# Kernel tuning notes

Measured on AMD Instinct MI355X. Metric: run time of the kernel, lower is better.

## Reference

```python
import jax, jax.numpy as jnp
import numpy as np

D_MODEL, N_LAYERS, NUM_CLASSES = 768, 4, 10
D_INNER = 2 * D_MODEL          # expand_factor=2
D_STATE = 16
D_CONV = 4
DT_RANK = (D_MODEL + 15) // 16  # ceil(d_model/16) = 48
B, L = 8, 2048
EPS = 1e-5


def setup_inputs() -> dict:
    key = jax.random.key(0)
    ks = jax.random.split(key, 16)
    s = 0.02
    inp = {
        'x': jax.random.normal(ks[0], (B, L, D_MODEL), jnp.float32),
        'labels': jax.random.randint(ks[1], (B,), 0, NUM_CLASSES, jnp.int64),
        # stacked per-layer params
        'in_proj_w': jax.random.normal(ks[2], (N_LAYERS, 2 * D_INNER, D_MODEL), jnp.float32) * s,
        'conv_w': jax.random.normal(ks[3], (N_LAYERS, D_INNER, 1, D_CONV), jnp.float32) * s,
        'conv_b': jnp.zeros((N_LAYERS, D_INNER), jnp.float32),
        'x_proj_w': jax.random.normal(ks[4], (N_LAYERS, DT_RANK + 2 * D_STATE, D_INNER), jnp.float32) * s,
        'dt_w': jax.random.normal(ks[5], (N_LAYERS, D_INNER, DT_RANK), jnp.float32) * s,
        'dt_b': jax.random.uniform(ks[6], (N_LAYERS, D_INNER), jnp.float32, -4.0, -2.0),
        'A_log': jnp.broadcast_to(jnp.log(jnp.arange(1, D_STATE + 1, dtype=jnp.float32)),
                                  (N_LAYERS, D_INNER, D_STATE)).copy(),
        'D_param': jnp.ones((N_LAYERS, D_INNER), jnp.float32),
        'out_proj_w': jax.random.normal(ks[7], (N_LAYERS, D_MODEL, D_INNER), jnp.float32) * s,
        'norm_w': jnp.ones((N_LAYERS, D_MODEL), jnp.float32),
        'normf_w': jnp.ones((D_MODEL,), jnp.float32),
        'cls_w': jax.random.normal(ks[8], (NUM_CLASSES, D_MODEL), jnp.float32) * s,
        'cls_b': jnp.zeros((NUM_CLASSES,), jnp.float32),
    }
    return inp


def rmsnorm(x, w):
    return x * jax.lax.rsqrt(jnp.mean(x * x, axis=-1, keepdims=True) + EPS) * w


def causal_dw_conv1d(x, w, b):
    # x: (B, L, ED), w: (ED, 1, K) depthwise, causal left padding
    y = jax.lax.conv_general_dilated(
        x.swapaxes(1, 2), w, window_strides=(1,), padding=[(D_CONV - 1, 0)],
        feature_group_count=D_INNER, dimension_numbers=('NCH', 'OIH', 'NCH'))
    return (y + b[:, None]).swapaxes(1, 2)


def selective_scan(xin, delta, Bm, Cm, A, Dp):
    # xin/delta: (B,L,ED), Bm/Cm: (B,L,N), A: (ED,N), Dp: (ED,)
    def step(h, t):
        d_t, B_t, C_t, x_t = t                      # (B,ED),(B,N),(B,N),(B,ED)
        dA = jnp.exp(d_t[..., None] * A)            # (B,ED,N)
        dBx = (d_t * x_t)[..., None] * B_t[:, None, :]
        h = dA * h + dBx
        y = jnp.einsum('ben,bn->be', h, C_t)
        return h, y

    h0 = jnp.zeros((xin.shape[0], D_INNER, D_STATE), xin.dtype)
    xs = (delta.swapaxes(0, 1), Bm.swapaxes(0, 1), Cm.swapaxes(0, 1), xin.swapaxes(0, 1))
    _, ys = jax.lax.scan(step, h0, xs)              # ys: (L,B,ED)
    return ys.swapaxes(0, 1) + xin * Dp


def mamba_block(x, in_w, cw, cb, xw, dtw, dtb, A_log, Dp, ow):
    xz = jnp.einsum('bld,ed->ble', x, in_w)         # (B,L,2*ED)
    xin, z = jnp.split(xz, 2, axis=-1)
    xin = jax.nn.silu(causal_dw_conv1d(xin, cw, cb))
    dbc = jnp.einsum('ble,fe->blf', xin, xw)
    delta_r = dbc[..., :DT_RANK]
    Bm = dbc[..., DT_RANK:DT_RANK + D_STATE]
    Cm = dbc[..., DT_RANK + D_STATE:]
    delta = jax.nn.softplus(jnp.einsum('blr,er->ble', delta_r, dtw) + dtb)
    A = -jnp.exp(A_log)
    y = selective_scan(xin, delta, Bm, Cm, A, Dp)
    y = y * jax.nn.silu(z)
    return jnp.einsum('ble,de->bld', y, ow)


def forward(x, labels, in_proj_w, conv_w, conv_b, x_proj_w, dt_w, dt_b,
            A_log, D_param, out_proj_w, norm_w, normf_w, cls_w, cls_b):
    h = x
    for i in range(N_LAYERS):
        h = h + mamba_block(rmsnorm(h, norm_w[i]), in_proj_w[i], conv_w[i], conv_b[i],
                            x_proj_w[i], dt_w[i], dt_b[i], A_log[i], D_param[i], out_proj_w[i])
    h = rmsnorm(h, normf_w)
    pooled = jnp.mean(h, axis=1)                    # (B, d_model)
    logits = pooled @ cls_w.T + cls_b               # (B, num_classes)
    logp = jax.nn.log_softmax(logits, axis=-1)
    loss = -jnp.mean(jnp.take_along_axis(logp, labels[:, None], axis=-1))
    return logits, loss


def reference(x, labels, in_proj_w, conv_w, conv_b, x_proj_w, dt_w, dt_b,
              A_log, D_param, out_proj_w, norm_w, normf_w, cls_w, cls_b):
    return forward(x, labels, in_proj_w, conv_w, conv_b, x_proj_w, dt_w, dt_b,
                   A_log, D_param, out_proj_w, norm_w, normf_w, cls_w, cls_b)
```

## Files before the change

### kernel.cpp

```cpp
#include <hip/hip_runtime.h>
#include <hip/hip_bf16.h>
#include <math.h>

#define MTOK 16384
#define DM   768
#define DI   1536
#define DS   16
#define RNK  48
#define LSEQ 2048
#define NBATCH 8
#define EPSV 1e-5f
#define CHK  16
#define CLEN (LSEQ / CHK)
#define BM 128
#define BN 128
#define BK 32
#define KSPLIT 8
#define EPS_STRIDE 72

typedef __hip_bfloat16 bf16;
typedef __attribute__((ext_vector_type(8))) short short8;
typedef __attribute__((ext_vector_type(4))) float floatx4;

__device__ __forceinline__ float b2f(bf16 v){ return __bfloat162float(v); }
__device__ __forceinline__ bf16  f2b(float v){ return __float2bfloat16(v); }
__device__ __forceinline__ float u2f(unsigned short u){
    union { unsigned int i; float f; } v; v.i = ((unsigned int)u) << 16; return v.f;
}
__device__ __forceinline__ unsigned pack_bf2(float a, float b){
    bf16 ta = f2b(a), tb = f2b(b);
    return (unsigned)(*(unsigned short*)&ta) | ((unsigned)(*(unsigned short*)&tb) << 16);
}
__device__ __forceinline__ float silu_f(float x){
    return x * __builtin_amdgcn_rcpf(1.f + __expf(-x));
}
__device__ __forceinline__ void gload_lds16(const void* g, void* l) {
    __builtin_amdgcn_global_load_lds(
        (const __attribute__((address_space(1))) void*)g,
        (__attribute__((address_space(3))) void*)l, 16, 0, 0);
}

__global__ __launch_bounds__(256) void cvt_kernel(
    const float* __restrict__ x, bf16* __restrict__ h, int n)
{
    int i = (blockIdx.x * 256 + threadIdx.x) * 4;
    if (i < n) {
        const float4 v = *(const float4*)(x + i);
        uint2 o;
        o.x = pack_bf2(v.x, v.y);
        o.y = pack_bf2(v.z, v.w);
        *(uint2*)((unsigned short*)h + i) = o;
    }
}

__global__ __launch_bounds__(256) void rmsnorm_kernel(
    const bf16* __restrict__ in, const float* __restrict__ w,
    bf16* __restrict__ out, float* __restrict__ rs_out)
{
    const int row  = blockIdx.x * 4 + (threadIdx.x >> 6);
    const int lane = threadIdx.x & 63;
    const unsigned short* rp = (const unsigned short*)in + (size_t)row * DM + lane * 12;
    uint2 u0 = *(const uint2*)rp;
    uint2 u1 = *(const uint2*)(rp + 4);
    uint2 u2 = *(const uint2*)(rp + 8);
    unsigned us[6] = {u0.x, u0.y, u1.x, u1.y, u2.x, u2.y};
    float v[12];
    #pragma unroll
    for (int i = 0; i < 6; i++) {
        v[2*i]   = u2f((unsigned short)(us[i] & 0xffff));
        v[2*i+1] = u2f((unsigned short)(us[i] >> 16));
    }
    float s = 0.f;
    #pragma unroll
    for (int i = 0; i < 12; i++) s += v[i] * v[i];
    #pragma unroll
    for (int o = 32; o > 0; o >>= 1) s += __shfl_xor(s, o, 64);
    float rs = rsqrtf(s * (1.f/DM) + EPSV);
    if (rs_out && lane == 0) rs_out[row] = rs;
    if (out) {
        const float4 w0 = *(const float4*)(w + lane*12);
        const float4 w1 = *(const float4*)(w + lane*12 + 4);
        const float4 w2 = *(const float4*)(w + lane*12 + 8);
        unsigned short* op = (unsigned short*)out + (size_t)row * DM + lane * 12;
        uint2 o0, o1, o2;
        o0.x = pack_bf2(v[0]*rs*w0.x,  v[1]*rs*w0.y);
        o0.y = pack_bf2(v[2]*rs*w0.z,  v[3]*rs*w0.w);
        o1.x = pack_bf2(v[4]*rs*w1.x,  v[5]*rs*w1.y);
        o1.y = pack_bf2(v[6]*rs*w1.z,  v[7]*rs*w1.w);
        o2.x = pack_bf2(v[8]*rs*w2.x,  v[9]*rs*w2.y);
        o2.y = pack_bf2(v[10]*rs*w2.z, v[11]*rs*w2.w);
        *(uint2*)op       = o0;
        *(uint2*)(op + 4) = o1;
        *(uint2*)(op + 8) = o2;
    }
}

template<int MODE, int CONVA>
__global__ __launch_bounds__(256) void mgemm(
    const short* __restrict__ A, int lda,
    const short* __restrict__ W, int ldw,
    bf16* __restrict__ C, int ldc,
    int M, int N, int K,
    const float* __restrict__ cw, const float* __restrict__ cb,
    int ksteps_per_split)
{
    __shared__ __attribute__((aligned(16))) short As[BM*BK];
    __shared__ __attribute__((aligned(16))) short Bs[BN*BK];

    const int gx = gridDim.x;
    int lid = blockIdx.y * gx + blockIdx.x;
    {
        const int nwg = gx * gridDim.y;
        const int q = nwg >> 3, r = nwg & 7;
        const int xcd = lid & 7, slot = lid >> 3;
        lid = (xcd < r ? xcd * (q + 1) : r * (q + 1) + (xcd - r) * q) + slot;
    }
    const int bm = (lid / gx) * BM;
    const int bn = (lid % gx) * BN;

    const int tid = threadIdx.x;
    const int wave = tid >> 6;
    const int lane = tid & 63;
    const int wm = (wave & 1) * 64;
    const int wn = (wave >> 1) * 64;
    const int r15 = lane & 15;
    const int quad = lane >> 4;

    int kbeg = 0, kend = K;
    if (MODE == 4) {
        kbeg = blockIdx.z * ksteps_per_split * BK;
        kend = kbeg + ksteps_per_split * BK;
        if (kend > K) kend = K;
    }

    const int srow = wave*32 + (lane >> 2);
    const int swz = (lane & 3) ^ ((lane >> 3) & 3);
    int wr0 = bn + srow;      if (wr0 >= N) wr0 = N - 1;
    int wr1 = bn + srow + 16; if (wr1 >= N) wr1 = N - 1;

    floatx4 acc[4][4];
    const floatx4 zero = {0.f, 0.f, 0.f, 0.f};
    #pragma unroll
    for (int i = 0; i < 4; i++)
        #pragma unroll
        for (int j = 0; j < 4; j++) acc[i][j] = zero;

    const int kk = tid & 31;
    const int tg = tid >> 5;
    const int sA = CONVA ? quad : (quad ^ ((r15 >> 1) & 3));
    const int sB = quad ^ ((r15 >> 1) & 3);

    for (int k0 = kbeg; k0 < kend; k0 += BK) {
        if (CONVA) {
            int e = k0 + kk;
            float c0 = cw[e*4+0], c1 = cw[e*4+1], c2 = cw[e*4+2], c3 = cw[e*4+3];
            float cbe = cb[e];
            int g0 = bm + tg*16;
            const unsigned short* xp = (const unsigned short*)A + (size_t)g0 * lda + e;
            float p0 = 0.f, p1 = 0.f, p2 = 0.f;
            if ((g0 & (LSEQ-1)) != 0) {
                p0 = u2f(xp[-(ptrdiff_t)3*lda]);
                p1 = u2f(xp[-(ptrdiff_t)2*lda]);
                p2 = u2f(xp[-(ptrdiff_t)1*lda]);
            }
            #pragma unroll
            for (int i = 0; i < 16; i++) {
                float xt = u2f(xp[(size_t)i * lda]);
                float xv = silu_f(cbe + c0*p0 + c1*p1 + c2*p2 + c3*xt);
                p0 = p1; p1 = p2; p2 = xt;
                bf16 t = f2b(xv);
                As[(tg*16 + i)*BK + kk] = *(short*)&t;
            }
        } else {
            gload_lds16(A + (size_t)(bm + srow)      * lda + k0 + swz*8, &As[(wave*32)*BK]);
            gload_lds16(A + (size_t)(bm + srow + 16) * lda + k0 + swz*8, &As[(wave*32 + 16)*BK]);
        }
        gload_lds16(W + (size_t)wr0 * ldw + k0 + swz*8, &Bs[(wave*32)*BK]);
        gload_lds16(W + (size_t)wr1 * ldw + k0 + swz*8, &Bs[(wave*32 + 16)*BK]);
        __syncthreads();

        short8 af[4], bfr[4];
        #pragma unroll
        for (int i = 0; i < 4; i++) af[i]  = *(const short8*)&As[(wm + i*16 + r15)*BK + sA*8];
        #pragma unroll
        for (int i = 0; i < 4; i++) bfr[i] = *(const short8*)&Bs[(wn + i*16 + r15)*BK + sB*8];
        #pragma unroll
        for (int mt = 0; mt < 4; mt++)
            #pragma unroll
            for (int nt = 0; nt < 4; nt++)
                acc[mt][nt] = __builtin_amdgcn_mfma_f32_16x16x32_bf16(
                    af[mt], bfr[nt], acc[mt][nt], 0, 0, 0);
        __syncthreads();
    }

    if (MODE == 4) {
        float* Cf = (float*)C;
        #pragma unroll
        for (int nt = 0; nt < 4; nt++) {
            int n = bn + wn + nt*16 + r15;
            if (n >= N) continue;
            #pragma unroll
            for (int mt = 0; mt < 4; mt++)
                #pragma unroll
                for (int reg = 0; reg < 4; reg++) {
                    int m = bm + wm + mt*16 + quad*4 + reg;
                    atomicAdd(&Cf[(size_t)m * ldc + n], acc[mt][nt][reg]);
                }
        }
        return;
    }

    short* ep = ((wave & 2) ? Bs : As) + (wave & 1) * 1152;
    const int lr = lane >> 2;
    const int lc = lane & 3;
    #pragma unroll
    for (int mt = 0; mt < 4; mt++) {
        #pragma unroll
        for (int nt = 0; nt < 4; nt++)
            #pragma unroll
            for (int reg = 0; reg < 4; reg++) {
                bf16 t = f2b(acc[mt][nt][reg]);
                ep[(quad*4 + reg)*EPS_STRIDE + nt*16 + r15] = *(short*)&t;
            }
        short8 v0 = *(const short8*)&ep[lr*EPS_STRIDE + lc*16];
        short8 v1 = *(const short8*)&ep[lr*EPS_STRIDE + lc*16 + 8];
        int gm = bm + wm + mt*16 + lr;
        int gn = bn + wn + lc*16;
        if (gn < N) {
            bf16* cp = C + (size_t)gm * ldc + gn;
            if (MODE == 0) {
                *(short8*)cp       = v0;
                *(short8*)(cp + 8) = v1;
            } else {
                short8 c0 = *(const short8*)cp;
                short8 c1 = *(const short8*)(cp + 8);
                short8 o0, o1;
                #pragma unroll
                for (int j = 0; j < 8; j++) {
                    float cv0 = u2f((unsigned short)c0[j]);
                    float av0 = u2f((unsigned short)v0[j]);
                    float cv1 = u2f((unsigned short)c1[j]);
                    float av1 = u2f((unsigned short)v1[j]);
                    float r0 = (MODE == 2) ? (cv0 + av0) : (cv0 * silu_f(av0));
                    float r1 = (MODE == 2) ? (cv1 + av1) : (cv1 * silu_f(av1));
                    bf16 t0 = f2b(r0), t1 = f2b(r1);
                    o0[j] = *(short*)&t0;
                    o1[j] = *(short*)&t1;
                }
                *(short8*)cp       = o0;
                *(short8*)(cp + 8) = o1;
            }
        }
    }
}

template<int PASS>
__global__ __launch_bounds__(256) void scan_pass_kernel(
    bf16* __restrict__ xy,
    const bf16* __restrict__ dbc,
    const float* __restrict__ A_log,
    const float* __restrict__ Dp,
    const float* __restrict__ dtw,
    const float* __restrict__ dtb,
    const float* __restrict__ cw,
    const float* __restrict__ cb,
    float* __restrict__ hst,
    float* __restrict__ Ssum,
    unsigned short* __restrict__ bound)
{
    int e = (blockIdx.x % (DI/256)) * 256 + threadIdx.x;
    int b = (blockIdx.x / (DI/256)) & (NBATCH - 1);
    int c = blockIdx.x / ((DI/256) * NBATCH);
    int t0 = c * CLEN;

    float w[RNK];
    #pragma unroll
    for (int r = 0; r < RNK; r++) w[r] = dtw[e*RNK + r];
    float a[DS];
    #pragma unroll
    for (int n = 0; n < DS; n++) a[n] = -__expf(A_log[e*DS + n]);
    float c0 = cw[e*4+0], c1 = cw[e*4+1], c2 = cw[e*4+2], c3 = cw[e*4+3];
    float cbe = cb[e], dtbe = dtb[e], dpe = Dp[e];

    size_t sidx = ((size_t)(b*DI) + e) * CHK + c;
    float hh[DS];
    if (PASS == 1) {
        #pragma unroll
        for (int n = 0; n < DS; n++) hh[n] = 0.f;
    } else {
        #pragma unroll
        for (int n = 0; n < DS; n++) hh[n] = hst[sidx*DS + n];
    }

    unsigned short* xrow = (unsigned short*)(xy + ((size_t)(b*LSEQ) + t0) * DI + e);
    const unsigned short* drow = (const unsigned short*)(dbc + ((size_t)(b*LSEQ) + t0) * 80);

    unsigned short r0, r1, r2;
    if (PASS == 1) {
        if (c == 0) { r0 = 0; r1 = 0; r2 = 0; }
        else {
            r0 = xrow[-(ptrdiff_t)3*DI];
            r1 = xrow[-(ptrdiff_t)2*DI];
            r2 = xrow[-(ptrdiff_t)1*DI];
        }
        bound[sidx*4+0] = r0; bound[sidx*4+1] = r1; bound[sidx*4+2] = r2;
    } else {
        r0 = bound[sidx*4+0]; r1 = bound[sidx*4+1]; r2 = bound[sidx*4+2];
    }
    float p0 = u2f(r0), p1 = u2f(r1), p2 = u2f(r2);

    float S = 0.f;
    for (int t = 0; t < CLEN; t++) {
        float xt = u2f(xrow[(size_t)t * DI]);
        float xv = silu_f(cbe + c0*p0 + c1*p1 + c2*p2 + c3*xt);
        p0 = p1; p1 = p2; p2 = xt;

        uint4 q[5];
        const uint4* d4 = (const uint4*)(drow + (size_t)t * 80);
        #pragma unroll
        for (int i = 0; i < 5; i++) q[i] = d4[i];
        uint4 q2[5];
        #pragma unroll
        for (int i = 0; i < 5; i++) q2[i] = d4[5 + i];
        const unsigned short* ds = (const unsigned short*)q;
        const unsigned short* ds2 = (const unsigned short*)q2;

        float acc = dtbe;
        #pragma unroll
        for (int r = 0; r < RNK; r++) acc += w[r] * u2f(ds[r]);
        float d = (acc > 20.f) ? acc : __logf(1.f + __expf(acc));
        float dx = d * xv;
        #pragma unroll
        for (int n = 0; n < DS; n++)
            hh[n] = __expf(d * a[n]) * hh[n] + dx * u2f(ds[RNK + n]);

        if (PASS == 1) {
            S += d;
        } else {
            float y = xv * dpe;
            #pragma unroll
            for (int n = 0; n < DS; n++) y += hh[n] * u2f(ds2[n]);
            bf16 yb = f2b(y);
            xrow[(size_t)t * DI] = *(unsigned short*)&yb;
        }
    }
    if (PASS == 1) {
        #pragma unroll
        for (int n = 0; n < DS; n++) hst[sidx*DS + n] = hh[n];
        Ssum[sidx] = S;
    }
}

__global__ __launch_bounds__(256) void scan_combine_kernel(
    float* __restrict__ hst, const float* __restrict__ Ssum,
    const float* __restrict__ A_log)
{
    int tid = blockIdx.x * 256 + threadIdx.x;
    int n = tid & 15;
    int bee = tid >> 4;
    int e = bee % DI;
    float a = -__expf(A_log[e*DS + n]);
    float run = 0.f;
    for (int c = 0; c < CHK; c++) {
        size_t idx = ((size_t)bee * CHK + c) * DS + n;
        float tmp = hst[idx];
        hst[idx] = run;
        run = tmp + __expf(a * Ssum[(size_t)bee*CHK + c]) * run;
    }
}

__global__ __launch_bounds__(128) void pool_kernel(
    const bf16* __restrict__ h, const float* __restrict__ rs,
    const float* __restrict__ wf, float* __restrict__ pooled)
{
    int b = blockIdx.x, dc = blockIdx.y, tc = blockIdx.z;
    int d = dc * 128 + threadIdx.x;
    float s = 0.f;
    int t0 = tc * 128;
    for (int t = t0; t < t0 + 128; t++) {
        int row = b * LSEQ + t;
        s += b2f(h[(size_t)row * DM + d]) * rs[row];
    }
    atomicAdd(&pooled[b * DM + d], s * wf[d] * (1.f / LSEQ));
}

__global__ __launch_bounds__(128) void head_kernel(
    const float* __restrict__ pooled, const float* __restrict__ cls_w,
    const float* __restrict__ cls_b, const int* __restrict__ labels,
    float* __restrict__ out)
{
    __shared__ float lg[80];
    int tid = threadIdx.x;
    if (tid < 80) {
        int b = tid / 10, c = tid % 10;
        float s = cls_b[c];
        for (int d = 0; d < DM; d++) s += pooled[b * DM + d] * cls_w[c * DM + d];
        lg[tid] = s;
    }
    __syncthreads();
    if (tid == 0) {
        float loss = 0.f;
        for (int b = 0; b < NBATCH; b++) {
            float mx = -1e30f;
            for (int c = 0; c < 10; c++) mx = fmaxf(mx, lg[b*10+c]);
            float se = 0.f;
            for (int c = 0; c < 10; c++) se += expf(lg[b*10+c] - mx);
            float lse = mx + logf(se);
            loss -= (lg[b*10 + labels[b]] - lse);
            for (int c = 0; c < 10; c++) out[b*10+c] = lg[b*10+c];
        }
        out[80] = loss / NBATCH;
    }
}

extern "C" void kernel_launch(void* const* d_in, const int* in_sizes, int n_in,
                              void* d_out, int out_size, void* d_ws, size_t ws_size,
                              hipStream_t stream) {
    const float* x          = (const float*)d_in[0];
    const int*   labels     = (const int*)d_in[1];
    const float* in_proj_w  = (const float*)d_in[2];
    const float* conv_w     = (const float*)d_in[3];
    const float* conv_b     = (const float*)d_in[4];
    const float* x_proj_w   = (const float*)d_in[5];
    const float* dt_w       = (const float*)d_in[6];
    const float* dt_b       = (const float*)d_in[7];
    const float* A_log      = (const float*)d_in[8];
    const float* D_param    = (const float*)d_in[9];
    const float* out_proj_w = (const float*)d_in[10];
    const float* norm_w     = (const float*)d_in[11];
    const float* normf_w    = (const float*)d_in[12];
    const float* cls_w      = (const float*)d_in[13];
    const float* cls_b      = (const float*)d_in[14];
    float* out = (float*)d_out;

    char* p = (char*)d_ws;
    bf16* h   = (bf16*)p;                 p += (size_t)MTOK * DM * 2;
    bf16* xn  = (bf16*)p;                 p += (size_t)MTOK * DM * 2;
    bf16* xy  = (bf16*)p;                 p += (size_t)MTOK * DI * 2;
    bf16* dbc = (bf16*)p;                 p += (size_t)MTOK * 80 * 2;
    float* dbcf = (float*)p;              p += (size_t)MTOK * 80 * 4;
    float* hst = (float*)p;               p += (size_t)NBATCH*DI*CHK*DS*4;
    float* Ssum = (float*)p;              p += (size_t)NBATCH*DI*CHK*4;
    unsigned short* bound = (unsigned short*)p; p += (size_t)NBATCH*DI*CHK*4*2;
    float* rsb    = (float*)p;            p += (size_t)MTOK * 4;
    float* pooled = (float*)p;            p += NBATCH * DM * 4;
    short* inw_b = (short*)p;             p += (size_t)2*DI*DM * 2;
    short* xw_b  = (short*)p;             p += (size_t)80*DI * 2;
    short* ow_b  = (short*)p;             p += (size_t)DM*DI * 2;

    cvt_kernel<<<(MTOK * DM) / 1024, 256, 0, stream>>>(x, h, MTOK * DM);
    hipMemsetAsync(pooled, 0, NBATCH * DM * sizeof(float), stream);

    int scan_grid = (DI/256) * NBATCH * CHK;

    for (int l = 0; l < 4; l++) {
        const float* inw = in_proj_w + (size_t)l * 2 * DI * DM;
        const float* cwl = conv_w + (size_t)l * DI * 4;
        const float* cbl = conv_b + (size_t)l * DI;
        const float* xwl = x_proj_w + (size_t)l * (RNK + 2*DS) * DI;
        const float* dwl = dt_w + (size_t)l * DI * RNK;
        const float* dbl = dt_b + (size_t)l * DI;
        const float* All = A_log + (size_t)l * DI * DS;
        const float* Dpl = D_param + (size_t)l * DI;
        const float* owl = out_proj_w + (size_t)l * DM * DI;

        cvt_kernel<<<(2*DI*DM)/1024, 256, 0, stream>>>(inw, (bf16*)inw_b, 2*DI*DM);
        cvt_kernel<<<(80*DI)/1024, 256, 0, stream>>>(xwl, (bf16*)xw_b, 80*DI);
        cvt_kernel<<<(DM*DI)/1024, 256, 0, stream>>>(owl, (bf16*)ow_b, DM*DI);

        rmsnorm_kernel<<<MTOK/4, 256, 0, stream>>>(h, norm_w + (size_t)l * DM, xn, nullptr);

        hipMemsetAsync(dbcf, 0, (size_t)MTOK * 80 * sizeof(float), stream);

        mgemm<0,0><<<dim3(DI/BN, MTOK/BM), 256, 0, stream>>>(
            (const short*)xn, DM, inw_b, DM, xy, DI, MTOK, DI, DM, nullptr, nullptr, 0);

        mgemm<4,1><<<dim3(1, MTOK/BM, KSPLIT), 256, 0, stream>>>(
            (const short*)xy, DI, xw_b, DI, (bf16*)dbcf, 80, MTOK, 80, DI,
            cwl, cbl, (DI/BK)/KSPLIT);
        cvt_kernel<<<(MTOK*80)/1024, 256, 0, stream>>>(dbcf, dbc, MTOK*80);

        scan_pass_kernel<1><<<scan_grid, 256, 0, stream>>>(
            xy, dbc, All, Dpl, dwl, dbl, cwl, cbl, hst, Ssum, bound);
        scan_combine_kernel<<<(NBATCH*DI*DS)/256, 256, 0, stream>>>(hst, Ssum, All);
        scan_pass_kernel<2><<<scan_grid, 256, 0, stream>>>(
            xy, dbc, All, Dpl, dwl, dbl, cwl, cbl, hst, Ssum, bound);

        mgemm<3,0><<<dim3(DI/BN, MTOK/BM), 256, 0, stream>>>(
            (const short*)xn, DM, inw_b + (size_t)DI*DM, DM, xy, DI, MTOK, DI, DM,
            nullptr, nullptr, 0);

        mgemm<2,0><<<dim3(DM/BN, MTOK/BM), 256, 0, stream>>>(
            (const short*)xy, DI, ow_b, DI, h, DM, MTOK, DM, DI, nullptr, nullptr, 0);
    }

    rmsnorm_kernel<<<MTOK/4, 256, 0, stream>>>(h, normf_w, nullptr, rsb);
    pool_kernel<<<dim3(NBATCH, DM/128, LSEQ/128), 128, 0, stream>>>(h, rsb, normf_w, pooled);
    head_kernel<<<1, 128, 0, stream>>>(pooled, cls_w, cls_b, labels, out);
}
```

Baseline: 1.192 ms.

## Use 256x256 double-buffered 8-wave MFMA GEMM for in/out projections

Replaces the 128x128 single-buffered GEMM used for the in_proj halves and out_proj with a 512-thread, 256x256-tile kernel. It double-buffers 64-wide K slices in 128KB of LDS, prefetches the next tile while issuing MFMAs, and uses explicit waitcnt, barriers and setprio for scheduling. The conv-fused split-K x_proj path is split out into its own unchanged kernel. The aim is more data reuse per tile and load/compute overlap, at the cost of a large LDS footprint and fewer workgroups in flight. The out_proj grid is only 3 tiles wide.

```diff
diff --git a/kernel.cpp b/kernel.cpp
--- a/kernel.cpp
+++ b/kernel.cpp
@@ -95,17 +95,14 @@
     }
 }
 
-template<int MODE, int CONVA>
-__global__ __launch_bounds__(256) void mgemm(
+template<int MODE>
+__global__ __launch_bounds__(512, 2) void mgemm8(
     const short* __restrict__ A, int lda,
     const short* __restrict__ W, int ldw,
     bf16* __restrict__ C, int ldc,
-    int M, int N, int K,
-    const float* __restrict__ cw, const float* __restrict__ cb,
-    int ksteps_per_split)
-{
-    __shared__ __attribute__((aligned(16))) short As[BM*BK];
-    __shared__ __attribute__((aligned(16))) short Bs[BN*BK];
+    int M, int N, int K)
+{
+    __shared__ __attribute__((aligned(16))) short lds8[65536];
 
     const int gx = gridDim.x;
     int lid = blockIdx.y * gx + blockIdx.x;
@@ -115,117 +112,163 @@
         const int xcd = lid & 7, slot = lid >> 3;
         lid = (xcd < r ? xcd * (q + 1) : r * (q + 1) + (xcd - r) * q) + slot;
     }
-    const int bm = (lid / gx) * BM;
-    const int bn = (lid % gx) * BN;
-
-    const int tid = threadIdx.x;
+    const int bm = (lid / gx) * 256;
+    const int bn = (lid % gx) * 256;
+
+    const int tid  = threadIdx.x;
     const int wave = tid >> 6;
     const int lane = tid & 63;
-    const int wm = (wave & 1) * 64;
-    const int wn = (wave >> 1) * 64;
-    const int r15 = lane & 15;
+    const int wr   = wave >> 2;
+    const int wc   = wave & 3;
+    const int r15  = lane & 15;
     const int quad = lane >> 4;
 
-    int kbeg = 0, kend = K;
-    if (MODE == 4) {
-        kbeg = blockIdx.z * ksteps_per_split * BK;
-        kend = kbeg + ksteps_per_split * BK;
-        if (kend > K) kend = K;
-    }
-
-    const int srow = wave*32 + (lane >> 2);
-    const int swz = (lane & 3) ^ ((lane >> 3) & 3);
-    int wr0 = bn + srow;      if (wr0 >= N) wr0 = N - 1;
-    int wr1 = bn + srow + 16; if (wr1 >= N) wr1 = N - 1;
-
-    floatx4 acc[4][4];
+    const int sp = (tid & 7) ^ ((tid >> 3) & 7);
+    const int rr = 2 * (tid >> 3) + (sp >> 2);
+    const int cc = (sp & 3) * 8;
+    const size_t gA = (size_t)(bm + rr) * lda + cc;
+    const size_t gB = (size_t)(bn + rr) * ldw + cc;
+    const int stW = wave * 512;
+
+    const int pp = ((quad) | ((r15 & 1) << 2)) ^ ((r15 >> 1) & 7);
+    const int laneA = (64 * wr + (r15 >> 1)) * 64 + pp * 8;
+    const int laneB = (32 * wc + (r15 >> 1)) * 64 + pp * 8;
+
+    floatx4 acc[8][4];
     const floatx4 zero = {0.f, 0.f, 0.f, 0.f};
     #pragma unroll
-    for (int i = 0; i < 4; i++)
+    for (int i = 0; i < 8; i++)
         #pragma unroll
         for (int j = 0; j < 4; j++) acc[i][j] = zero;
 
-    const int kk = tid & 31;
-    const int tg = tid >> 5;
-    const int sA = CONVA ? quad : (quad ^ ((r15 >> 1) & 3));
-    const int sB = quad ^ ((r15 >> 1) & 3);
-
-    for (int k0 = kbeg; k0 < kend; k0 += BK) {
-        if (CONVA) {
-            int e = k0 + kk;
-            float c0 = cw[e*4+0], c1 = cw[e*4+1], c2 = cw[e*4+2], c3 = cw[e*4+3];
-            float cbe = cb[e];
-            int g0 = bm + tg*16;
-            const unsigned short* xp = (const unsigned short*)A + (size_t)g0 * lda + e;
-            float p0 = 0.f, p1 = 0.f, p2 = 0.f;
-            if ((g0 & (LSEQ-1)) != 0) {
-                p0 = u2f(xp[-(ptrdiff_t)3*lda]);
-                p1 = u2f(xp[-(ptrdiff_t)2*lda]);
-                p2 = u2f(xp[-(ptrdiff_t)1*lda]);
-            }
-            #pragma unroll
-            for (int i = 0; i < 16; i++) {
-                float xt = u2f(xp[(size_t)i * lda]);
-                float xv = silu_f(cbe + c0*p0 + c1*p1 + c2*p2 + c3*xt);
-                p0 = p1; p1 = p2; p2 = xt;
-                bf16 t = f2b(xv);
-                As[(tg*16 + i)*BK + kk] = *(short*)&t;
-            }
-        } else {
-            gload_lds16(A + (size_t)(bm + srow)      * lda + k0 + swz*8, &As[(wave*32)*BK]);
-            gload_lds16(A + (size_t)(bm + srow + 16) * lda + k0 + swz*8, &As[(wave*32 + 16)*BK]);
-        }
-        gload_lds16(W + (size_t)wr0 * ldw + k0 + swz*8, &Bs[(wave*32)*BK]);
-        gload_lds16(W + (size_t)wr1 * ldw + k0 + swz*8, &Bs[(wave*32 + 16)*BK]);
-        __syncthreads();
-
-        short8 af[4], bfr[4];
-        #pragma unroll
-        for (int i = 0; i < 4; i++) af[i]  = *(const short8*)&As[(wm + i*16 + r15)*BK + sA*8];
-        #pragma unroll
-        for (int i = 0; i < 4; i++) bfr[i] = *(const short8*)&Bs[(wn + i*16 + r15)*BK + sB*8];
-        #pragma unroll
-        for (int mt = 0; mt < 4; mt++)
-            #pragma unroll
-            for (int nt = 0; nt < 4; nt++)
-                acc[mt][nt] = __builtin_amdgcn_mfma_f32_16x16x32_bf16(
-                    af[mt], bfr[nt], acc[mt][nt], 0, 0, 0);
-        __syncthreads();
-    }
-
-    if (MODE == 4) {
-        float* Cf = (float*)C;
-        #pragma unroll
-        for (int nt = 0; nt < 4; nt++) {
-            int n = bn + wn + nt*16 + r15;
-            if (n >= N) continue;
-            #pragma unroll
-            for (int mt = 0; mt < 4; mt++)
-                #pragma unroll
-                for (int reg = 0; reg < 4; reg++) {
-                    int m = bm + wm + mt*16 + quad*4 + reg;
-                    atomicAdd(&Cf[(size_t)m * ldc + n], acc[mt][nt][reg]);
-                }
-        }
-        return;
-    }
-
-    short* ep = ((wave & 2) ? Bs : As) + (wave & 1) * 1152;
+    const int NT = K / 64;
+
+    auto stageA = [&](int ks, int buf, int kt) {
+        const int reg = buf * 32768 + ks * 8192;
+        const size_t kb = (size_t)kt * 64 + ks * 32;
+        gload_lds16(A + gA + kb,                     &lds8[reg + stW]);
+        gload_lds16(A + gA + kb + (size_t)128 * lda, &lds8[reg + 4096 + stW]);
+    };
+    auto stageB = [&](int ks, int buf, int kt) {
+        const int reg = buf * 32768 + 16384 + ks * 8192;
+        const size_t kb = (size_t)kt * 64 + ks * 32;
+        gload_lds16(W + gB + kb,                     &lds8[reg + stW]);
+        gload_lds16(W + gB + kb + (size_t)128 * ldw, &lds8[reg + 4096 + stW]);
+    };
+
+    stageB(0, 0, 0); stageA(0, 0, 0); stageB(1, 0, 0); stageA(1, 0, 0);
+    asm volatile("s_waitcnt vmcnt(4)" ::: "memory");
+    __builtin_amdgcn_s_barrier();
+    __builtin_amdgcn_sched_barrier(0);
+
+    for (int t = 0; t < NT; ++t) {
+        const int cb = (t & 1) * 32768;
+        const int nb = (t + 1) & 1;
+        const bool st = (t + 1 < NT);
+        short8 bfv[4], afA[4], afB[4];
+
+        #pragma unroll
+        for (int nf = 0; nf < 4; nf++)
+            bfv[nf] = *(const short8*)&lds8[cb + 16384 + laneB + nf*512];
+        #pragma unroll
+        for (int m = 0; m < 4; m++)
+            afA[m] = *(const short8*)&lds8[cb + laneA + m*512];
+        if (st) stageB(0, nb, t + 1);
+        __builtin_amdgcn_sched_barrier(0);
+        __builtin_amdgcn_s_barrier();
+        asm volatile("s_waitcnt lgkmcnt(0)" ::: "memory");
+        __builtin_amdgcn_sched_barrier(0);
+        __builtin_amdgcn_s_setprio(1);
+        #pragma unroll
+        for (int m = 0; m < 4; m++)
+            #pragma unroll
+            for (int nf = 0; nf < 4; nf++)
+                acc[m][nf] = __builtin_amdgcn_mfma_f32_16x16x32_bf16(
+                    afA[m], bfv[nf], acc[m][nf], 0, 0, 0);
+        __builtin_amdgcn_s_setprio(0);
+        __builtin_amdgcn_sched_barrier(0);
+        __builtin_amdgcn_s_barrier();
+
+        #pragma unroll
+        for (int m = 0; m < 4; m++)
+            afB[m] = *(const short8*)&lds8[cb + laneA + (m+4)*512];
+        if (st) stageA(0, nb, t + 1);
+        __builtin_amdgcn_sched_barrier(0);
+        if (st) asm volatile("s_waitcnt vmcnt(4)" ::: "memory");
+        else    asm volatile("s_waitcnt vmcnt(0)" ::: "memory");
+        __builtin_amdgcn_s_barrier();
+        asm volatile("s_waitcnt lgkmcnt(0)" ::: "memory");
+        __builtin_amdgcn_sched_barrier(0);
+        __builtin_amdgcn_s_setprio(1);
+        #pragma unroll
+        for (int m = 0; m < 4; m++)
+            #pragma unroll
+            for (int nf = 0; nf < 4; nf++)
+                acc[m+4][nf] = __builtin_amdgcn_mfma_f32_16x16x32_bf16(
+                    afB[m], bfv[nf], acc[m+4][nf], 0, 0, 0);
+        __builtin_amdgcn_s_setprio(0);
+        __builtin_amdgcn_sched_barrier(0);
+        __builtin_amdgcn_s_barrier();
+
+        #pragma unroll
+        for (int nf = 0; nf < 4; nf++)
+            bfv[nf] = *(const short8*)&lds8[cb + 24576 + laneB + nf*512];
+        #pragma unroll
+        for (int m = 0; m < 4; m++)
+            afA[m] = *(const short8*)&lds8[cb + 8192 + laneA + m*512];
+        if (st) stageB(1, nb, t + 1);
+        __builtin_amdgcn_sched_barrier(0);
+        __builtin_amdgcn_s_barrier();
+        asm volatile("s_waitcnt lgkmcnt(0)" ::: "memory");
+        __builtin_amdgcn_sched_barrier(0);
+        __builtin_amdgcn_s_setprio(1);
+        #pragma unroll
+        for (int m = 0; m < 4; m++)
+            #pragma unroll
+            for (int nf = 0; nf < 4; nf++)
+                acc[m][nf] = __builtin_amdgcn_mfma_f32_16x16x32_bf16(
+                    afA[m], bfv[nf], acc[m][nf], 0, 0, 0);
+        __builtin_amdgcn_s_setprio(0);
+        __builtin_amdgcn_sched_barrier(0);
+        __builtin_amdgcn_s_barrier();
+
+        #pragma unroll
+        for (int m = 0; m < 4; m++)
+            afB[m] = *(const short8*)&lds8[cb + 8192 + laneA + (m+4)*512];
+        if (st) stageA(1, nb, t + 1);
+        __builtin_amdgcn_sched_barrier(0);
+        if (st) asm volatile("s_waitcnt vmcnt(4)" ::: "memory");
+        __builtin_amdgcn_s_barrier();
+        asm volatile("s_waitcnt lgkmcnt(0)" ::: "memory");
+        __builtin_amdgcn_sched_barrier(0);
+        __builtin_amdgcn_s_setprio(1);
+        #pragma unroll
+        for (int m = 0; m < 4; m++)
+            #pragma unroll
+            for (int nf = 0; nf < 4; nf++)
+                acc[m+4][nf] = __builtin_amdgcn_mfma_f32_16x16x32_bf16(
+                    afB[m], bfv[nf], acc[m+4][nf], 0, 0, 0);
+        __builtin_amdgcn_s_setprio(0);
+        __builtin_amdgcn_sched_barrier(0);
+        __builtin_amdgcn_s_barrier();
+    }
+
+    short* ep = lds8 + wave * 1152;
     const int lr = lane >> 2;
     const int lc = lane & 3;
     #pragma unroll
-    for (int mt = 0; mt < 4; mt++) {
-        #pragma unroll
-        for (int nt = 0; nt < 4; nt++)
+    for (int mt = 0; mt < 8; mt++) {
+        #pragma unroll
+        for (int nf = 0; nf < 4; nf++)
             #pragma unroll
             for (int reg = 0; reg < 4; reg++) {
-                bf16 t = f2b(acc[mt][nt][reg]);
-                ep[(quad*4 + reg)*EPS_STRIDE + nt*16 + r15] = *(short*)&t;
+                bf16 tt = f2b(acc[mt][nf][reg]);
+                ep[(quad*4 + reg)*EPS_STRIDE + nf*16 + r15] = *(short*)&tt;
             }
         short8 v0 = *(const short8*)&ep[lr*EPS_STRIDE + lc*16];
         short8 v1 = *(const short8*)&ep[lr*EPS_STRIDE + lc*16 + 8];
-        int gm = bm + wm + mt*16 + lr;
-        int gn = bn + wn + lc*16;
+        int gm = bm + wr*128 + mt*16 + lr;
+        int gn = bn + wc*64 + lc*16;
         if (gn < N) {
             bf16* cp = C + (size_t)gm * ldc + gn;
             if (MODE == 0) {
@@ -241,9 +284,9 @@
                     float av0 = u2f((unsigned short)v0[j]);
                     float cv1 = u2f((unsigned short)c1[j]);
                     float av1 = u2f((unsigned short)v1[j]);
-                    float r0 = (MODE == 2) ? (cv0 + av0) : (cv0 * silu_f(av0));
-                    float r1 = (MODE == 2) ? (cv1 + av1) : (cv1 * silu_f(av1));
-                    bf16 t0 = f2b(r0), t1 = f2b(r1);
+                    float rr0 = (MODE == 2) ? (cv0 + av0) : (cv0 * silu_f(av0));
+                    float rr1 = (MODE == 2) ? (cv1 + av1) : (cv1 * silu_f(av1));
+                    bf16 t0 = f2b(rr0), t1 = f2b(rr1);
                     o0[j] = *(short*)&t0;
                     o1[j] = *(short*)&t1;
                 }
@@ -251,6 +294,111 @@
                 *(short8*)(cp + 8) = o1;
             }
         }
+    }
+}
+
+__global__ __launch_bounds__(256) void mgemm_conv(
+    const short* __restrict__ A, int lda,
+    const short* __restrict__ W, int ldw,
+    float* __restrict__ Cf, int ldc,
+    int M, int N, int K,
+    const float* __restrict__ cw, const float* __restrict__ cb,
+    int ksteps_per_split)
+{
+    __shared__ __attribute__((aligned(16))) short As[BM*BK];
+    __shared__ __attribute__((aligned(16))) short Bs[BN*BK];
+
+    const int gx = gridDim.x;
+    int lid = blockIdx.y * gx + blockIdx.x;
+    {
+        const int nwg = gx * gridDim.y;
+        const int q = nwg >> 3, r = nwg & 7;
+        const int xcd = lid & 7, slot = lid >> 3;
+        lid = (xcd < r ? xcd * (q + 1) : r * (q + 1) + (xcd - r) * q) + slot;
+    }
+    const int bm = (lid / gx) * BM;
+    const int bn = (lid % gx) * BN;
+
+    const int tid = threadIdx.x;
+    const int wave = tid >> 6;
+    const int lane = tid & 63;
+    const int wm = (wave & 1) * 64;
+    const int wn = (wave >> 1) * 64;
+    const int r15 = lane & 15;
+    const int quad = lane >> 4;
+
+    int kbeg = blockIdx.z * ksteps_per_split * BK;
+    int kend = kbeg + ksteps_per_split * BK;
+    if (kend > K) kend = K;
+
+    const int srow = wave*32 + (lane >> 2);
+    const int swz = (lane & 3) ^ ((lane >> 3) & 3);
+    int wr0 = bn + srow;      if (wr0 >= N) wr0 = N - 1;
+    int wr1 = bn + srow + 16; if (wr1 >= N) wr1 = N - 1;
+
+    floatx4 acc[4][4];
+    const floatx4 zero = {0.f, 0.f, 0.f, 0.f};
+    #pragma unroll
+    for (int i = 0; i < 4; i++)
+        #pragma unroll
+        for (int j = 0; j < 4; j++) acc[i][j] = zero;
+
+    const int kk = tid & 31;
+    const int tg = tid >> 5;
+    const int sA = quad;
+    const int sB = quad ^ ((r15 >> 1) & 3);
+
+    for (int k0 = kbeg; k0 < kend; k0 += BK) {
+        {
+            int e = k0 + kk;
+            float c0 = cw[e*4+0], c1 = cw[e*4+1], c2 = cw[e*4+2], c3 = cw[e*4+3];
+            float cbe = cb[e];
+            int g0 = bm + tg*16;
+            const unsigned short* xp = (const unsigned short*)A + (size_t)g0 * lda + e;
+            float p0 = 0.f, p1 = 0.f, p2 = 0.f;
+            if ((g0 & (LSEQ-1)) != 0) {
+                p0 = u2f(xp[-(ptrdiff_t)3*lda]);
+                p1 = u2f(xp[-(ptrdiff_t)2*lda]);
+                p2 = u2f(xp[-(ptrdiff_t)1*lda]);
+            }
+            #pragma unroll
+            for (int i = 0; i < 16; i++) {
+                float xt = u2f(xp[(size_t)i * lda]);
+                float xv = silu_f(cbe + c0*p0 + c1*p1 + c2*p2 + c3*xt);
+                p0 = p1; p1 = p2; p2 = xt;
+                bf16 t = f2b(xv);
+                As[(tg*16 + i)*BK + kk] = *(short*)&t;
+            }
+        }
+        gload_lds16(W + (size_t)wr0 * ldw + k0 + swz*8, &Bs[(wave*32)*BK]);
+        gload_lds16(W + (size_t)wr1 * ldw + k0 + swz*8, &Bs[(wave*32 + 16)*BK]);
+        __syncthreads();
+
+        short8 af[4], bfr[4];
+        #pragma unroll
+        for (int i = 0; i < 4; i++) af[i]  = *(const short8*)&As[(wm + i*16 + r15)*BK + sA*8];
+        #pragma unroll
+        for (int i = 0; i < 4; i++) bfr[i] = *(const short8*)&Bs[(wn + i*16 + r15)*BK + sB*8];
+        #pragma unroll
+        for (int mt = 0; mt < 4; mt++)
+            #pragma unroll
+            for (int nt = 0; nt < 4; nt++)
+                acc[mt][nt] = __builtin_amdgcn_mfma_f32_16x16x32_bf16(
+                    af[mt], bfr[nt], acc[mt][nt], 0, 0, 0);
+        __syncthreads();
+    }
+
+    #pragma unroll
+    for (int nt = 0; nt < 4; nt++) {
+        int n = bn + wn + nt*16 + r15;
+        if (n >= N) continue;
+        #pragma unroll
+        for (int mt = 0; mt < 4; mt++)
+            #pragma unroll
+            for (int reg = 0; reg < 4; reg++) {
+                int m = bm + wm + mt*16 + quad*4 + reg;
+                atomicAdd(&Cf[(size_t)m * ldc + n], acc[mt][nt][reg]);
+            }
     }
 }
 
@@ -472,11 +620,11 @@
 
         hipMemsetAsync(dbcf, 0, (size_t)MTOK * 80 * sizeof(float), stream);
 
-        mgemm<0,0><<<dim3(DI/BN, MTOK/BM), 256, 0, stream>>>(
-            (const short*)xn, DM, inw_b, DM, xy, DI, MTOK, DI, DM, nullptr, nullptr, 0);
-
-        mgemm<4,1><<<dim3(1, MTOK/BM, KSPLIT), 256, 0, stream>>>(
-            (const short*)xy, DI, xw_b, DI, (bf16*)dbcf, 80, MTOK, 80, DI,
+        mgemm8<0><<<dim3(DI/256, MTOK/256), 512, 0, stream>>>(
+            (const short*)xn, DM, inw_b, DM, xy, DI, MTOK, DI, DM);
+
+        mgemm_conv<<<dim3(1, MTOK/BM, KSPLIT), 256, 0, stream>>>(
+            (const short*)xy, DI, xw_b, DI, dbcf, 80, MTOK, 80, DI,
             cwl, cbl, (DI/BK)/KSPLIT);
         cvt_kernel<<<(MTOK*80)/1024, 256, 0, stream>>>(dbcf, dbc, MTOK*80);
 
@@ -486,12 +634,11 @@
         scan_pass_kernel<2><<<scan_grid, 256, 0, stream>>>(
             xy, dbc, All, Dpl, dwl, dbl, cwl, cbl, hst, Ssum, bound);
 
-        mgemm<3,0><<<dim3(DI/BN, MTOK/BM), 256, 0, stream>>>(
-            (const short*)xn, DM, inw_b + (size_t)DI*DM, DM, xy, DI, MTOK, DI, DM,
-            nullptr, nullptr, 0);
-
-        mgemm<2,0><<<dim3(DM/BN, MTOK/BM), 256, 0, stream>>>(
-            (const short*)xy, DI, ow_b, DI, h, DM, MTOK, DM, DI, nullptr, nullptr, 0);
+        mgemm8<3><<<dim3(DI/256, MTOK/256), 512, 0, stream>>>(
+            (const short*)xn, DM, inw_b + (size_t)DI*DM, DM, xy, DI, MTOK, DI, DM);
+
+        mgemm8<2><<<dim3(DM/256, MTOK/256), 512, 0, stream>>>(
+            (const short*)xy, DI, ow_b, DI, h, DM, MTOK, DM, DI);
     }
 
     rmsnorm_kernel<<<MTOK/4, 256, 0, stream>>>(h, normf_w, nullptr, rsb);
```

New measurement: 1.167 ms. 2.1% less time.

## Triple-buffer GEMM LDS pipeline and fuse z-projection with gating into scan

Applied to the files above, without the earlier changes.

The main bf16 GEMM now uses a three-stage LDS ring with async global-to-LDS prefetch two k-steps ahead. Each step waits on vmcnt and a single barrier instead of two __syncthreads, and MFMA work runs at raised priority. When the workspace is large enough, the in_proj GEMM computes both the x and z halves in one launch into an interleaved buffer. The scan's second pass then applies the silu(z) gate, which removes the separate gated GEMM pass. This trades more LDS per block, and so possibly lower occupancy, for overlapped loads. It also adds a workspace-size-dependent code path.

```diff
diff --git a/kernel.cpp b/kernel.cpp
--- a/kernel.cpp
+++ b/kernel.cpp
@@ -95,17 +95,14 @@
     }
 }
 
-template<int MODE, int CONVA>
+template<int MODE>
 __global__ __launch_bounds__(256) void mgemm(
     const short* __restrict__ A, int lda,
     const short* __restrict__ W, int ldw,
     bf16* __restrict__ C, int ldc,
-    int M, int N, int K,
-    const float* __restrict__ cw, const float* __restrict__ cb,
-    int ksteps_per_split)
-{
-    __shared__ __attribute__((aligned(16))) short As[BM*BK];
-    __shared__ __attribute__((aligned(16))) short Bs[BN*BK];
+    int M, int N, int K)
+{
+    __shared__ __attribute__((aligned(16))) short lds[3 * 8192];
 
     const int gx = gridDim.x;
     int lid = blockIdx.y * gx + blockIdx.x;
@@ -126,18 +123,20 @@
     const int r15 = lane & 15;
     const int quad = lane >> 4;
 
-    int kbeg = 0, kend = K;
-    if (MODE == 4) {
-        kbeg = blockIdx.z * ksteps_per_split * BK;
-        kend = kbeg + ksteps_per_split * BK;
-        if (kend > K) kend = K;
-    }
-
     const int srow = wave*32 + (lane >> 2);
     const int swz = (lane & 3) ^ ((lane >> 3) & 3);
     int wr0 = bn + srow;      if (wr0 >= N) wr0 = N - 1;
     int wr1 = bn + srow + 16; if (wr1 >= N) wr1 = N - 1;
 
+    const short* Ab  = A + (size_t)(bm + srow) * lda + swz*8;
+    const short* Ab1 = A + (size_t)(bm + srow + 16) * lda + swz*8;
+    const short* Wb0 = W + (size_t)wr0 * ldw + swz*8;
+    const short* Wb1 = W + (size_t)wr1 * ldw + swz*8;
+    const int dA0 = (wave*32)*BK;
+    const int dA1 = (wave*32 + 16)*BK;
+    const int dB0 = 4096 + (wave*32)*BK;
+    const int dB1 = 4096 + (wave*32 + 16)*BK;
+
     floatx4 acc[4][4];
     const floatx4 zero = {0.f, 0.f, 0.f, 0.f};
     #pragma unroll
@@ -145,72 +144,53 @@
         #pragma unroll
         for (int j = 0; j < 4; j++) acc[i][j] = zero;
 
-    const int kk = tid & 31;
-    const int tg = tid >> 5;
-    const int sA = CONVA ? quad : (quad ^ ((r15 >> 1) & 3));
-    const int sB = quad ^ ((r15 >> 1) & 3);
-
-    for (int k0 = kbeg; k0 < kend; k0 += BK) {
-        if (CONVA) {
-            int e = k0 + kk;
-            float c0 = cw[e*4+0], c1 = cw[e*4+1], c2 = cw[e*4+2], c3 = cw[e*4+3];
-            float cbe = cb[e];
-            int g0 = bm + tg*16;
-            const unsigned short* xp = (const unsigned short*)A + (size_t)g0 * lda + e;
-            float p0 = 0.f, p1 = 0.f, p2 = 0.f;
-            if ((g0 & (LSEQ-1)) != 0) {
-                p0 = u2f(xp[-(ptrdiff_t)3*lda]);
-                p1 = u2f(xp[-(ptrdiff_t)2*lda]);
-                p2 = u2f(xp[-(ptrdiff_t)1*lda]);
-            }
-            #pragma unroll
-            for (int i = 0; i < 16; i++) {
-                float xt = u2f(xp[(size_t)i * lda]);
-                float xv = silu_f(cbe + c0*p0 + c1*p1 + c2*p2 + c3*xt);
-                p0 = p1; p1 = p2; p2 = xt;
-                bf16 t = f2b(xv);
-                As[(tg*16 + i)*BK + kk] = *(short*)&t;
-            }
-        } else {
-            gload_lds16(A + (size_t)(bm + srow)      * lda + k0 + swz*8, &As[(wave*32)*BK]);
-            gload_lds16(A + (size_t)(bm + srow + 16) * lda + k0 + swz*8, &As[(wave*32 + 16)*BK]);
-        }
-        gload_lds16(W + (size_t)wr0 * ldw + k0 + swz*8, &Bs[(wave*32)*BK]);
-        gload_lds16(W + (size_t)wr1 * ldw + k0 + swz*8, &Bs[(wave*32 + 16)*BK]);
-        __syncthreads();
+    const int sA = quad ^ ((r15 >> 1) & 3);
+    const int sB = sA;
+
+    const int NK = K / BK;
+
+    auto STAGE = [&](int buf, int kt) {
+        const int bb = buf * 8192;
+        const size_t kc = (size_t)kt * BK;
+        gload_lds16(Ab  + kc, &lds[bb + dA0]);
+        gload_lds16(Ab1 + kc, &lds[bb + dA1]);
+        gload_lds16(Wb0 + kc, &lds[bb + dB0]);
+        gload_lds16(Wb1 + kc, &lds[bb + dB1]);
+    };
+
+    STAGE(0, 0); STAGE(1, 1);
+    asm volatile("s_waitcnt vmcnt(4)" ::: "memory");
+    __builtin_amdgcn_s_barrier();
+    __builtin_amdgcn_sched_barrier(0);
+
+    for (int t = 0; t < NK; ++t) {
+        const short* As = &lds[(t % 3) * 8192];
+        const short* Bs = As + 4096;
 
         short8 af[4], bfr[4];
         #pragma unroll
         for (int i = 0; i < 4; i++) af[i]  = *(const short8*)&As[(wm + i*16 + r15)*BK + sA*8];
         #pragma unroll
         for (int i = 0; i < 4; i++) bfr[i] = *(const short8*)&Bs[(wn + i*16 + r15)*BK + sB*8];
+
+        if (t + 2 < NK) STAGE((t + 2) % 3, t + 2);
+
+        __builtin_amdgcn_s_setprio(1);
         #pragma unroll
         for (int mt = 0; mt < 4; mt++)
             #pragma unroll
             for (int nt = 0; nt < 4; nt++)
                 acc[mt][nt] = __builtin_amdgcn_mfma_f32_16x16x32_bf16(
                     af[mt], bfr[nt], acc[mt][nt], 0, 0, 0);
-        __syncthreads();
-    }
-
-    if (MODE == 4) {
-        float* Cf = (float*)C;
-        #pragma unroll
-        for (int nt = 0; nt < 4; nt++) {
-            int n = bn + wn + nt*16 + r15;
-            if (n >= N) continue;
-            #pragma unroll
-            for (int mt = 0; mt < 4; mt++)
-                #pragma unroll
-                for (int reg = 0; reg < 4; reg++) {
-                    int m = bm + wm + mt*16 + quad*4 + reg;
-                    atomicAdd(&Cf[(size_t)m * ldc + n], acc[mt][nt][reg]);
-                }
-        }
-        return;
-    }
-
-    short* ep = ((wave & 2) ? Bs : As) + (wave & 1) * 1152;
+        __builtin_amdgcn_s_setprio(0);
+
+        if (t + 2 < NK)      asm volatile("s_waitcnt vmcnt(4)" ::: "memory");
+        else if (t + 1 < NK) asm volatile("s_waitcnt vmcnt(0)" ::: "memory");
+        __builtin_amdgcn_s_barrier();
+        __builtin_amdgcn_sched_barrier(0);
+    }
+
+    short* ep = lds + ((wave & 2) ? 4096 : 0) + (wave & 1) * 1152;
     const int lr = lane >> 2;
     const int lc = lane & 3;
     #pragma unroll
@@ -254,9 +234,114 @@
     }
 }
 
+__global__ __launch_bounds__(256) void mgemm_conv(
+    const short* __restrict__ A, int lda,
+    const short* __restrict__ W, int ldw,
+    float* __restrict__ Cf, int ldc,
+    int M, int N, int K,
+    const float* __restrict__ cw, const float* __restrict__ cb,
+    int ksteps_per_split)
+{
+    __shared__ __attribute__((aligned(16))) short As[BM*BK];
+    __shared__ __attribute__((aligned(16))) short Bs[BN*BK];
+
+    const int gx = gridDim.x;
+    int lid = blockIdx.y * gx + blockIdx.x;
+    {
+        const int nwg = gx * gridDim.y;
+        const int q = nwg >> 3, r = nwg & 7;
+        const int xcd = lid & 7, slot = lid >> 3;
+        lid = (xcd < r ? xcd * (q + 1) : r * (q + 1) + (xcd - r) * q) + slot;
+    }
+    const int bm = (lid / gx) * BM;
+    const int bn = (lid % gx) * BN;
+
+    const int tid = threadIdx.x;
+    const int wave = tid >> 6;
+    const int lane = tid & 63;
+    const int wm = (wave & 1) * 64;
+    const int wn = (wave >> 1) * 64;
+    const int r15 = lane & 15;
+    const int quad = lane >> 4;
+
+    int kbeg = blockIdx.z * ksteps_per_split * BK;
+    int kend = kbeg + ksteps_per_split * BK;
+    if (kend > K) kend = K;
+
+    const int srow = wave*32 + (lane >> 2);
+    const int swz = (lane & 3) ^ ((lane >> 3) & 3);
+    int wr0 = bn + srow;      if (wr0 >= N) wr0 = N - 1;
+    int wr1 = bn + srow + 16; if (wr1 >= N) wr1 = N - 1;
+
+    floatx4 acc[4][4];
+    const floatx4 zero = {0.f, 0.f, 0.f, 0.f};
+    #pragma unroll
+    for (int i = 0; i < 4; i++)
+        #pragma unroll
+        for (int j = 0; j < 4; j++) acc[i][j] = zero;
+
+    const int kk = tid & 31;
+    const int tg = tid >> 5;
+    const int sA = quad;
+    const int sB = quad ^ ((r15 >> 1) & 3);
+
+    for (int k0 = kbeg; k0 < kend; k0 += BK) {
+        {
+            int e = k0 + kk;
+            float c0 = cw[e*4+0], c1 = cw[e*4+1], c2 = cw[e*4+2], c3 = cw[e*4+3];
+            float cbe = cb[e];
+            int g0 = bm + tg*16;
+            const unsigned short* xp = (const unsigned short*)A + (size_t)g0 * lda + e;
+            float p0 = 0.f, p1 = 0.f, p2 = 0.f;
+            if ((g0 & (LSEQ-1)) != 0) {
+                p0 = u2f(xp[-(ptrdiff_t)3*lda]);
+                p1 = u2f(xp[-(ptrdiff_t)2*lda]);
+                p2 = u2f(xp[-(ptrdiff_t)1*lda]);
+            }
+            #pragma unroll
+            for (int i = 0; i < 16; i++) {
+                float xt = u2f(xp[(size_t)i * lda]);
+                float xv = silu_f(cbe + c0*p0 + c1*p1 + c2*p2 + c3*xt);
+                p0 = p1; p1 = p2; p2 = xt;
+                bf16 t = f2b(xv);
+                As[(tg*16 + i)*BK + kk] = *(short*)&t;
+            }
+        }
+        gload_lds16(W + (size_t)wr0 * ldw + k0 + swz*8, &Bs[(wave*32)*BK]);
+        gload_lds16(W + (size_t)wr1 * ldw + k0 + swz*8, &Bs[(wave*32 + 16)*BK]);
+        __syncthreads();
+
+        short8 af[4], bfr[4];
+        #pragma unroll
+        for (int i = 0; i < 4; i++) af[i]  = *(const short8*)&As[(wm + i*16 + r15)*BK + sA*8];
+        #pragma unroll
+        for (int i = 0; i < 4; i++) bfr[i] = *(const short8*)&Bs[(wn + i*16 + r15)*BK + sB*8];
+        #pragma unroll
+        for (int mt = 0; mt < 4; mt++)
+            #pragma unroll
+            for (int nt = 0; nt < 4; nt++)
+                acc[mt][nt] = __builtin_amdgcn_mfma_f32_16x16x32_bf16(
+                    af[mt], bfr[nt], acc[mt][nt], 0, 0, 0);
+        __syncthreads();
+    }
+
+    #pragma unroll
+    for (int nt = 0; nt < 4; nt++) {
+        int n = bn + wn + nt*16 + r15;
+        if (n >= N) continue;
+        #pragma unroll
+        for (int mt = 0; mt < 4; mt++)
+            #pragma unroll
+            for (int reg = 0; reg < 4; reg++) {
+                int m = bm + wm + mt*16 + quad*4 + reg;
+                atomicAdd(&Cf[(size_t)m * ldc + n], acc[mt][nt][reg]);
+            }
+    }
+}
+
 template<int PASS>
 __global__ __launch_bounds__(256) void scan_pass_kernel(
-    bf16* __restrict__ xy,
+    bf16* __restrict__ xy, int xld, int gate,
     const bf16* __restrict__ dbc,
     const float* __restrict__ A_log,
     const float* __restrict__ Dp,
@@ -292,16 +377,16 @@
         for (int n = 0; n < DS; n++) hh[n] = hst[sidx*DS + n];
     }
 
-    unsigned short* xrow = (unsigned short*)(xy + ((size_t)(b*LSEQ) + t0) * DI + e);
+    unsigned short* xrow = (unsigned short*)xy + ((size_t)(b*LSEQ) + t0) * xld + e;
     const unsigned short* drow = (const unsigned short*)(dbc + ((size_t)(b*LSEQ) + t0) * 80);
 
     unsigned short r0, r1, r2;
     if (PASS == 1) {
         if (c == 0) { r0 = 0; r1 = 0; r2 = 0; }
         else {
-            r0 = xrow[-(ptrdiff_t)3*DI];
-            r1 = xrow[-(ptrdiff_t)2*DI];
-            r2 = xrow[-(ptrdiff_t)1*DI];
+            r0 = xrow[-(ptrdiff_t)3*xld];
+            r1 = xrow[-(ptrdiff_t)2*xld];
+            r2 = xrow[-(ptrdiff_t)1*xld];
         }
         bound[sidx*4+0] = r0; bound[sidx*4+1] = r1; bound[sidx*4+2] = r2;
     } else {
@@ -311,7 +396,7 @@
 
     float S = 0.f;
     for (int t = 0; t < CLEN; t++) {
-        float xt = u2f(xrow[(size_t)t * DI]);
+        float xt = u2f(xrow[(size_t)t * xld]);
         float xv = silu_f(cbe + c0*p0 + c1*p1 + c2*p2 + c3*xt);
         p0 = p1; p1 = p2; p2 = xt;
 
@@ -340,8 +425,12 @@
             float y = xv * dpe;
             #pragma unroll
             for (int n = 0; n < DS; n++) y += hh[n] * u2f(ds2[n]);
+            if (gate) {
+                float zt = u2f(xrow[(size_t)t * xld + 1536]);
+                y *= silu_f(zt);
+            }
             bf16 yb = f2b(y);
-            xrow[(size_t)t * DI] = *(unsigned short*)&yb;
+            xrow[(size_t)t * xld] = *(unsigned short*)&yb;
         }
     }
     if (PASS == 1) {
@@ -433,10 +522,19 @@
     const float* cls_b      = (const float*)d_in[14];
     float* out = (float*)d_out;
 
+    const size_t fixed = (size_t)MTOK*DM*2*2
+                       + (size_t)MTOK*80*2 + (size_t)MTOK*80*4
+                       + (size_t)NBATCH*DI*CHK*DS*4 + (size_t)NBATCH*DI*CHK*4
+                       + (size_t)NBATCH*DI*CHK*4*2
+                       + (size_t)MTOK*4 + (size_t)NBATCH*DM*4
+                       + (size_t)2*DI*DM*2 + (size_t)80*DI*2 + (size_t)DM*DI*2;
+    const int fused = (ws_size >= fixed + (size_t)MTOK * (2*DI) * 2 + 1024) ? 1 : 0;
+    const int XLD = fused ? 2*DI : DI;
+
     char* p = (char*)d_ws;
     bf16* h   = (bf16*)p;                 p += (size_t)MTOK * DM * 2;
     bf16* xn  = (bf16*)p;                 p += (size_t)MTOK * DM * 2;
-    bf16* xy  = (bf16*)p;                 p += (size_t)MTOK * DI * 2;
+    bf16* xz  = (bf16*)p;                 p += (size_t)MTOK * XLD * 2;
     bf16* dbc = (bf16*)p;                 p += (size_t)MTOK * 80 * 2;
     float* dbcf = (float*)p;              p += (size_t)MTOK * 80 * 4;
     float* hst = (float*)p;               p += (size_t)NBATCH*DI*CHK*DS*4;
@@ -472,26 +570,32 @@
 
         hipMemsetAsync(dbcf, 0, (size_t)MTOK * 80 * sizeof(float), stream);
 
-        mgemm<0,0><<<dim3(DI/BN, MTOK/BM), 256, 0, stream>>>(
-            (const short*)xn, DM, inw_b, DM, xy, DI, MTOK, DI, DM, nullptr, nullptr, 0);
-
-        mgemm<4,1><<<dim3(1, MTOK/BM, KSPLIT), 256, 0, stream>>>(
-            (const short*)xy, DI, xw_b, DI, (bf16*)dbcf, 80, MTOK, 80, DI,
+        if (fused) {
+            mgemm<0><<<dim3(2*DI/BN, MTOK/BM), 256, 0, stream>>>(
+                (const short*)xn, DM, inw_b, DM, xz, XLD, MTOK, 2*DI, DM);
+        } else {
+            mgemm<0><<<dim3(DI/BN, MTOK/BM), 256, 0, stream>>>(
+                (const short*)xn, DM, inw_b, DM, xz, XLD, MTOK, DI, DM);
+        }
+
+        mgemm_conv<<<dim3(1, MTOK/BM, KSPLIT), 256, 0, stream>>>(
+            (const short*)xz, XLD, xw_b, DI, dbcf, 80, MTOK, 80, DI,
             cwl, cbl, (DI/BK)/KSPLIT);
         cvt_kernel<<<(MTOK*80)/1024, 256, 0, stream>>>(dbcf, dbc, MTOK*80);
 
         scan_pass_kernel<1><<<scan_grid, 256, 0, stream>>>(
-            xy, dbc, All, Dpl, dwl, dbl, cwl, cbl, hst, Ssum, bound);
+            xz, XLD, 0, dbc, All, Dpl, dwl, dbl, cwl, cbl, hst, Ssum, bound);
         scan_combine_kernel<<<(NBATCH*DI*DS)/256, 256, 0, stream>>>(hst, Ssum, All);
         scan_pass_kernel<2><<<scan_grid, 256, 0, stream>>>(
-            xy, dbc, All, Dpl, dwl, dbl, cwl, cbl, hst, Ssum, bound);
-
-        mgemm<3,0><<<dim3(DI/BN, MTOK/BM), 256, 0, stream>>>(
-            (const short*)xn, DM, inw_b + (size_t)DI*DM, DM, xy, DI, MTOK, DI, DM,
-            nullptr, nullptr, 0);
-
-        mgemm<2,0><<<dim3(DM/BN, MTOK/BM), 256, 0, stream>>>(
-            (const short*)xy, DI, ow_b, DI, h, DM, MTOK, DM, DI, nullptr, nullptr, 0);
+            xz, XLD, fused, dbc, All, Dpl, dwl, dbl, cwl, cbl, hst, Ssum, bound);
+
+        if (!fused) {
+            mgemm<3><<<dim3(DI/BN, MTOK/BM), 256, 0, stream>>>(
+                (const short*)xn, DM, inw_b + (size_t)DI*DM, DM, xz, XLD, MTOK, DI, DM);
+        }
+
+        mgemm<2><<<dim3(DM/BN, MTOK/BM), 256, 0, stream>>>(
+            (const short*)xz, XLD, ow_b, DI, h, DM, MTOK, DM, DI);
     }
 
     rmsnorm_kernel<<<MTOK/4, 256, 0, stream>>>(h, normf_w, nullptr, rsb);
```

Result: faster. 1.113 ms (-6.7%).
